# Optimization experiments

Measured on AMD Instinct MI355X. Metric: run time of the kernel, lower is better.

Reference implementation:

```python
import jax, jax.numpy as jnp
import numpy as np

H = 8          # head_num
DK = 16        # qkv_dim
CLIP = 10.0    # logit clipping


def _heads(x):
    # (b, n, H*DK) -> (b, H, n, DK)
    b, n, _ = x.shape
    return x.reshape(b, n, H, DK).transpose(0, 2, 1, 3)


def setup_inputs() -> dict:
    key = jax.random.key(0)
    ks = jax.random.split(key, 10)
    batch, problem, d, klen = 2048, 100, 128, 10
    s = 1.0 / np.sqrt(d)
    problems = jax.random.uniform(ks[0], (batch, problem, 2), dtype=jnp.float32)
    encoded_nodes = jax.random.normal(ks[1], (batch, problem, d), dtype=jnp.float32)
    Wq_first = jax.random.normal(ks[2], (d, H * DK), dtype=jnp.float32) * s
    Wq_last = jax.random.normal(ks[3], (d, H * DK), dtype=jnp.float32) * s
    Wk = jax.random.normal(ks[4], (d, H * DK), dtype=jnp.float32) * s
    Wv = jax.random.normal(ks[5], (d, H * DK), dtype=jnp.float32) * s
    Wcomb = jax.random.normal(ks[6], (H * DK, d), dtype=jnp.float32) * s
    # prefix: k distinct node indices per batch row (first k of a random permutation)
    perm = jax.vmap(lambda kk: jax.random.permutation(kk, problem))(
        jax.random.split(ks[7], batch))
    prefix = perm[:, :klen].astype(jnp.int32)
    return {"problems": problems, "encoded_nodes": encoded_nodes,
            "Wq_first": Wq_first, "Wq_last": Wq_last, "Wk": Wk, "Wv": Wv,
            "Wcomb": Wcomb, "prefix": prefix}


def reference(problems, encoded_nodes, Wq_first, Wq_last, Wk, Wv, Wcomb, prefix):
    batch, problem, d = encoded_nodes.shape
    b_idx = jnp.arange(batch)
    sqrt_dk = jnp.sqrt(jnp.float32(DK))
    sqrt_d = jnp.sqrt(jnp.float32(d))

    # set_kv: precompute multi-head K, V once (single-head key = encoded_nodes)
    kh = _heads(encoded_nodes @ Wk)   # (b, H, n, DK)
    vh = _heads(encoded_nodes @ Wv)   # (b, H, n, DK)

    # set_q1: query contribution of the first node (last node of prefix)
    last0 = prefix[:, -1]
    q1 = _heads(encoded_nodes[b_idx, last0][:, None, :] @ Wq_first)  # (b, H, 1, DK)

    # visited mask from prefix
    visited0 = jnp.zeros((batch, problem), dtype=bool)
    visited0 = visited0.at[b_idx[:, None], prefix].set(True)

    def step(carry, _):
        visited, cur = carry
        enc_last = encoded_nodes[b_idx, cur][:, None, :]            # (b, 1, d)
        q = q1 + _heads(enc_last @ Wq_last)                         # (b, H, 1, DK)
        ninf = jnp.where(visited, -jnp.inf, 0.0)                    # (b, n)
        scores = jnp.einsum('bhqe,bhne->bhqn', q, kh) / sqrt_dk
        att = jax.nn.softmax(scores + ninf[:, None, None, :], axis=-1)
        mh = jnp.einsum('bhqn,bhne->bhqe', att, vh)                 # (b, H, 1, DK)
        mh = mh.transpose(0, 2, 1, 3).reshape(batch, 1, H * DK) @ Wcomb  # (b, 1, d)
        sc = jnp.einsum('bqd,bnd->bqn', mh, encoded_nodes)[:, 0] / sqrt_d  # (b, n)
        logits = CLIP * jnp.tanh(sc) + ninf
        sel = jnp.argmax(logits, axis=-1)                           # (b,)
        visited = visited.at[b_idx, sel].set(True)
        return (visited, sel), sel

    steps = problem - prefix.shape[1]
    _, sels = jax.lax.scan(step, (visited0, last0), None, length=steps)
    tour = jnp.concatenate([prefix, sels.T.astype(prefix.dtype)], axis=1)  # (b, problem)
    return tour
```

## Files before the change

### kernel.cpp

```cpp
#include <hip/hip_runtime.h>
#include <math.h>

#define N      100
#define D      128
#define KL     10
#define S0     90
#define STEPS  90
#define LDK    132
#define NT     512

__device__ __forceinline__ float dot4(float4 a, float4 b) {
  return a.x*b.x + a.y*b.y + a.z*b.z + a.w*b.w;
}
__device__ __forceinline__ void fma4(float4& acc, float a, float4 v) {
  acc.x += a*v.x; acc.y += a*v.y; acc.z += a*v.z; acc.w += a*v.w;
}

template<int RPT>
__device__ __forceinline__ void cc(const float* __restrict__ encB,
                                   const float* __restrict__ W,
                                   bool wRowMajor, int base, int cnt,
                                   const int* __restrict__ slotNode,
                                   float* __restrict__ stage, int tid) {
  const int col = tid & 127;
  const int grp = tid >> 7;
  float acc[RPT];
  int   nd [RPT];
  #pragma unroll
  for (int ii = 0; ii < RPT; ++ii) {
    acc[ii] = 0.f;
    int r = grp + 4*ii;
    nd[ii] = (r < cnt) ? __builtin_amdgcn_readfirstlane(slotNode[base + r]) : 0;
  }
  for (int dd = 0; dd < D; dd += 16) {
    float w[16];
    #pragma unroll
    for (int t = 0; t < 16; ++t)
      w[t] = wRowMajor ? W[col*D + dd + t] : W[(dd+t)*D + col];
    #pragma unroll
    for (int ii = 0; ii < RPT; ++ii) {
      int r = grp + 4*ii;
      if (r < cnt) {
        const float* er = encB + (size_t)nd[ii]*D + dd;
        float a0=0,a1=0,a2=0,a3=0;
        #pragma unroll
        for (int t = 0; t < 16; t += 4) {
          a0 += er[t]*w[t];   a1 += er[t+1]*w[t+1];
          a2 += er[t+2]*w[t+2]; a3 += er[t+3]*w[t+3];
        }
        acc[ii] += (a0+a1)+(a2+a3);
      }
    }
  }
  #pragma unroll
  for (int ii = 0; ii < RPT; ++ii) {
    int r = grp + 4*ii;
    if (r < cnt) stage[(base + r)*LDK + col] = acc[ii];
  }
}

__global__ __launch_bounds__(NT, 4)
void policy_kernel(const float* __restrict__ enc,
                   const float* __restrict__ Wq_first,
                   const float* __restrict__ Wq_last,
                   const float* __restrict__ Wk,
                   const float* __restrict__ Wv,
                   const float* __restrict__ Wcomb,
                   const int*   __restrict__ prefix,
                   int*         __restrict__ out) {
  __shared__ __align__(16) float sCE[S0*LDK];
  __shared__ __align__(16) float sq[D];
  __shared__ __align__(16) float sAtt[8*96];
  __shared__ __align__(16) float sMh[D];
  __shared__ float sSum[8];
  __shared__ int   sSlotNode[96];
  __shared__ unsigned long long sPacked[2];
  __shared__ int   sLast0;

  const int tid = threadIdx.x;
  const int b   = blockIdx.x;
  const float* encB = enc + (size_t)b*N*D;

  if (tid < KL) out[(size_t)b*N + tid] = prefix[b*KL + tid];
  if (tid < 48) sAtt[(tid/6)*96 + 90 + (tid%6)] = 0.f;
  if (tid == 0) {
    unsigned vis[4] = {0u,0u,0u,0u};
    const int* pr = prefix + b*KL;
    for (int j = 0; j < KL; ++j) { int n = pr[j]; vis[n>>5] |= 1u << (n&31); }
    int cnt = 0;
    for (int n = 0; n < N; ++n)
      if (!((vis[n>>5] >> (n&31)) & 1u)) sSlotNode[cnt++] = n;
    sLast0 = pr[KL-1];
    sPacked[0] = 0ull; sPacked[1] = 0ull;
  }
  __syncthreads();

  if (tid < D) {
    const int last0 = sLast0;
    const float* er = encB + (size_t)last0*D;
    float a0=0,a1=0,a2=0,a3=0;
    #pragma unroll
    for (int d = 0; d < D; d += 4) {
      a0 += er[d]  *Wq_first[d*D     + tid];
      a1 += er[d+1]*Wq_first[(d+1)*D + tid];
      a2 += er[d+2]*Wq_first[(d+2)*D + tid];
      a3 += er[d+3]*Wq_first[(d+3)*D + tid];
    }
    sMh[tid] = (a0+a1)+(a2+a3);
  }
  __syncthreads();

  const int col = tid & 127;
  const int grp = tid >> 7;
  float qp[23];
  {
    int nd[23];
    #pragma unroll
    for (int ii = 0; ii < 23; ++ii) {
      int r = grp + 4*ii;
      nd[ii] = (r < S0) ? __builtin_amdgcn_readfirstlane(sSlotNode[r])
                        : ((r == S0) ? sLast0 : 0);
      qp[ii] = 0.f;
    }
    for (int dd = 0; dd < D; dd += 16) {
      float w[16];
      #pragma unroll
      for (int t = 0; t < 16; ++t) w[t] = Wq_last[(dd+t)*D + col];
      #pragma unroll
      for (int ii = 0; ii < 23; ++ii) {
        int r = grp + 4*ii;
        if (r <= S0) {
          const float* er = encB + (size_t)nd[ii]*D + dd;
          float a0=0,a1=0,a2=0,a3=0;
          #pragma unroll
          for (int t = 0; t < 16; t += 4) {
            a0 += er[t]*w[t];   a1 += er[t+1]*w[t+1];
            a2 += er[t+2]*w[t+2]; a3 += er[t+3]*w[t+3];
          }
          qp[ii] += (a0+a1)+(a2+a3);
        }
      }
    }
    const float q1c = sMh[col];
    #pragma unroll
    for (int ii = 0; ii < 23; ++ii) qp[ii] += q1c;
  }

  const int h = tid >> 6, l = tid & 63;

  cc<23>(encB, Wk, false, 0, S0, sSlotNode, sCE, tid);
  __syncthreads();
  float4 ka0,ka1,ka2,ka3, kb0,kb1,kb2,kb3;
  {
    const float* p = &sCE[l*LDK + h*16];
    ka0 = *(const float4*)(p+0);  ka1 = *(const float4*)(p+4);
    ka2 = *(const float4*)(p+8);  ka3 = *(const float4*)(p+12);
  }
  if (l < 26) {
    const float* p = &sCE[(64+l)*LDK + h*16];
    kb0 = *(const float4*)(p+0);  kb1 = *(const float4*)(p+4);
    kb2 = *(const float4*)(p+8);  kb3 = *(const float4*)(p+12);
  } else {
    kb0=kb1=kb2=kb3 = make_float4(0.f,0.f,0.f,0.f);
  }
  __syncthreads();

  const int cQuad = tid >> 4;
  const int cStrm = tid & 15;
  const int ch    = cQuad >> 2;
  cc<12>(encB, Wv, false,  0, 48, sSlotNode, sCE, tid);
  cc<12>(encB, Wv, false, 48, 42, sSlotNode, sCE, tid);
  __syncthreads();
  float4 v0,v1,v2,v3,v4,v5;
  v0 = *(const float4*)&sCE[(cStrm     )*LDK + cQuad*4];
  v1 = *(const float4*)&sCE[(cStrm + 16)*LDK + cQuad*4];
  v2 = *(const float4*)&sCE[(cStrm + 32)*LDK + cQuad*4];
  v3 = *(const float4*)&sCE[(cStrm + 48)*LDK + cQuad*4];
  v4 = *(const float4*)&sCE[(cStrm + 64)*LDK + cQuad*4];
  v5 = (cStrm < 10) ? *(const float4*)&sCE[(cStrm + 80)*LDK + cQuad*4]
                    : make_float4(0.f,0.f,0.f,0.f);
  __syncthreads();

  cc<6>(encB, Wcomb, true,  0, 24, sSlotNode, sCE, tid);
  cc<6>(encB, Wcomb, true, 24, 24, sSlotNode, sCE, tid);
  cc<6>(encB, Wcomb, true, 48, 24, sSlotNode, sCE, tid);
  cc<6>(encB, Wcomb, true, 72, 18, sSlotNode, sCE, tid);
  if (grp == 2) sq[col] = qp[22];
  __syncthreads();

  const int di  = tid >> 2;
  const int dkc = tid & 3;
  float visA = 0.f, visB = 0.f, visD = 0.f;

  for (int step = 0; step < STEPS; ++step) {
    const int p = step & 1;

    {
      if (tid == NT-1) sPacked[p] = 0ull;
      const float4 q0 = *(const float4*)&sq[h*16 + 0];
      const float4 q1 = *(const float4*)&sq[h*16 + 4];
      const float4 q2 = *(const float4*)&sq[h*16 + 8];
      const float4 q3 = *(const float4*)&sq[h*16 + 12];
      float s0 = dot4(q0,ka0)+dot4(q1,ka1)+dot4(q2,ka2)+dot4(q3,ka3);
      float x0 = expf(s0*0.25f + visA);
      sAtt[h*96 + l] = x0;
      float x1 = 0.f;
      if (l < 26) {
        float s1 = dot4(q0,kb0)+dot4(q1,kb1)+dot4(q2,kb2)+dot4(q3,kb3);
        x1 = expf(s1*0.25f + visB);
        sAtt[h*96 + 64 + l] = x1;
      }
      float loc = x0 + x1;
      #pragma unroll
      for (int off = 32; off; off >>= 1) loc += __shfl_xor(loc, off);
      if (l == 0) sSum[h] = loc;
    }
    __syncthreads();

    {
      float4 acc = make_float4(0.f,0.f,0.f,0.f);
      fma4(acc, sAtt[ch*96 + cStrm     ], v0);
      fma4(acc, sAtt[ch*96 + cStrm + 16], v1);
      fma4(acc, sAtt[ch*96 + cStrm + 32], v2);
      fma4(acc, sAtt[ch*96 + cStrm + 48], v3);
      fma4(acc, sAtt[ch*96 + cStrm + 64], v4);
      fma4(acc, sAtt[ch*96 + cStrm + 80], v5);
      #pragma unroll
      for (int off = 1; off < 16; off <<= 1) {
        acc.x += __shfl_xor(acc.x, off);
        acc.y += __shfl_xor(acc.y, off);
        acc.z += __shfl_xor(acc.z, off);
        acc.w += __shfl_xor(acc.w, off);
      }
      if (cStrm == 0) {
        const float r = 1.0f / sSum[ch];
        float4 o; o.x=acc.x*r; o.y=acc.y*r; o.z=acc.z*r; o.w=acc.w*r;
        *(float4*)&sMh[cQuad*4] = o;
      }
    }
    __syncthreads();

    if (tid < 384) {
      float a = 0.f;
      #pragma unroll
      for (int j = 0; j < 8; ++j) {
        const float4 ce = *(const float4*)&sCE[di*LDK + dkc*32 + j*4];
        const float4 mh = *(const float4*)&sMh[dkc*32 + j*4];
        a += dot4(ce, mh);
      }
      a += __shfl_xor(a, 1);
      a += __shfl_xor(a, 2);
      float val = (di < S0) ? a + visD : -INFINITY;
      int   idx = (di < S0) ? di : 127;
      #pragma unroll
      for (int off = 32; off; off >>= 1) {
        float ov = __shfl_xor(val, off);
        int   oi = __shfl_xor(idx, off);
        if (ov > val || (ov == val && oi < idx)) { val = ov; idx = oi; }
      }
      if (l == 0) {
        unsigned s = __float_as_uint(val);
        s = (s & 0x80000000u) ? ~s : (s | 0x80000000u);
        unsigned long long pk = ((unsigned long long)s << 32)
                              | (unsigned long long)(unsigned)(127 - idx);
        atomicMax(&sPacked[p], pk);
      }
    }
    __syncthreads();

    {
      const unsigned long long u = sPacked[p];
      const int idx = __builtin_amdgcn_readfirstlane(127 - (int)(u & 0xFFull));
      if (tid == 0) out[(size_t)b*N + KL + step] = sSlotNode[idx];
      if (idx == l)      visA = -INFINITY;
      if (idx == l + 64) visB = -INFINITY;
      if (idx == di)     visD = -INFINITY;
      const int want = idx >> 2;
      float qv = qp[0];
      #pragma unroll
      for (int ii = 1; ii < 23; ++ii) qv = (want == ii) ? qp[ii] : qv;
      if (grp == (idx & 3)) sq[col] = qv;
    }
    __syncthreads();
  }
}

extern "C" void kernel_launch(void* const* d_in, const int* in_sizes, int n_in,
                              void* d_out, int out_size, void* d_ws, size_t ws_size,
                              hipStream_t stream) {
  const float* enc      = (const float*)d_in[1];
  const float* Wq_first = (const float*)d_in[2];
  const float* Wq_last  = (const float*)d_in[3];
  const float* Wk       = (const float*)d_in[4];
  const float* Wv       = (const float*)d_in[5];
  const float* Wcomb    = (const float*)d_in[6];
  const int*   prefix   = (const int*)d_in[7];
  const int batch = in_sizes[7] / KL;
  policy_kernel<<<batch, NT, 0, stream>>>(enc, Wq_first, Wq_last, Wk, Wv, Wcomb,
                                          prefix, (int*)d_out);
}
```

Before: 2.567 ms.

## Remap query ownership per wavefront and drop two block barriers per step

Query-projection columns are reassigned so that each wavefront computes and updates exactly the 16 query entries of its own head. The attention-weight sum and the query refresh can then rely on ordering within a wavefront, which removes the barrier after the softmax and the barrier at the end of each step. The reset of the argmax slot moves to the next step's buffer, the argmax shuffle skips lane offsets that are already reduced, and the select chain over saved queries becomes a switch. The cost is a dependence on intra-wave LDS ordering with no explicit fence, and a switch that may compile to branches or indexed register access.

```diff
diff --git a/kernel.cpp b/kernel.cpp
--- a/kernel.cpp
+++ b/kernel.cpp
@@ -110,25 +110,26 @@
   }
   __syncthreads();
 
-  const int col = tid & 127;
-  const int grp = tid >> 7;
+  const int h = tid >> 6, l = tid & 63;
+
+  const int qcol = (h << 4) | (l & 15);
+  const int qrg  = l >> 4;
   float qp[23];
   {
     int nd[23];
     #pragma unroll
     for (int ii = 0; ii < 23; ++ii) {
-      int r = grp + 4*ii;
-      nd[ii] = (r < S0) ? __builtin_amdgcn_readfirstlane(sSlotNode[r])
-                        : ((r == S0) ? sLast0 : 0);
+      int r = qrg + 4*ii;
+      nd[ii] = (r < S0) ? sSlotNode[r] : ((r == S0) ? sLast0 : 0);
       qp[ii] = 0.f;
     }
     for (int dd = 0; dd < D; dd += 16) {
       float w[16];
       #pragma unroll
-      for (int t = 0; t < 16; ++t) w[t] = Wq_last[(dd+t)*D + col];
+      for (int t = 0; t < 16; ++t) w[t] = Wq_last[(dd+t)*D + qcol];
       #pragma unroll
       for (int ii = 0; ii < 23; ++ii) {
-        int r = grp + 4*ii;
+        int r = qrg + 4*ii;
         if (r <= S0) {
           const float* er = encB + (size_t)nd[ii]*D + dd;
           float a0=0,a1=0,a2=0,a3=0;
@@ -141,12 +142,10 @@
         }
       }
     }
-    const float q1c = sMh[col];
+    const float q1c = sMh[qcol];
     #pragma unroll
     for (int ii = 0; ii < 23; ++ii) qp[ii] += q1c;
   }
-
-  const int h = tid >> 6, l = tid & 63;
 
   cc<23>(encB, Wk, false, 0, S0, sSlotNode, sCE, tid);
   __syncthreads();
@@ -185,7 +184,7 @@
   cc<6>(encB, Wcomb, true, 24, 24, sSlotNode, sCE, tid);
   cc<6>(encB, Wcomb, true, 48, 24, sSlotNode, sCE, tid);
   cc<6>(encB, Wcomb, true, 72, 18, sSlotNode, sCE, tid);
-  if (grp == 2) sq[col] = qp[22];
+  if (qrg == 2) sq[qcol] = qp[22];
   __syncthreads();
 
   const int di  = tid >> 2;
@@ -193,10 +192,7 @@
   float visA = 0.f, visB = 0.f, visD = 0.f;
 
   for (int step = 0; step < STEPS; ++step) {
-    const int p = step & 1;
-
     {
-      if (tid == NT-1) sPacked[p] = 0ull;
       const float4 q0 = *(const float4*)&sq[h*16 + 0];
       const float4 q1 = *(const float4*)&sq[h*16 + 4];
       const float4 q2 = *(const float4*)&sq[h*16 + 8];
@@ -215,7 +211,6 @@
       for (int off = 32; off; off >>= 1) loc += __shfl_xor(loc, off);
       if (l == 0) sSum[h] = loc;
     }
-    __syncthreads();
 
     {
       float4 acc = make_float4(0.f,0.f,0.f,0.f);
@@ -240,6 +235,8 @@
     }
     __syncthreads();
 
+    if (tid == NT-1) sPacked[(step+1)&1] = 0ull;
+
     if (tid < 384) {
       float a = 0.f;
       #pragma unroll
@@ -253,7 +250,7 @@
       float val = (di < S0) ? a + visD : -INFINITY;
       int   idx = (di < S0) ? di : 127;
       #pragma unroll
-      for (int off = 32; off; off >>= 1) {
+      for (int off = 4; off <= 32; off <<= 1) {
         float ov = __shfl_xor(val, off);
         int   oi = __shfl_xor(idx, off);
         if (ov > val || (ov == val && oi < idx)) { val = ov; idx = oi; }
@@ -263,25 +260,47 @@
         s = (s & 0x80000000u) ? ~s : (s | 0x80000000u);
         unsigned long long pk = ((unsigned long long)s << 32)
                               | (unsigned long long)(unsigned)(127 - idx);
-        atomicMax(&sPacked[p], pk);
+        atomicMax(&sPacked[step&1], pk);
       }
     }
     __syncthreads();
 
     {
-      const unsigned long long u = sPacked[p];
+      const unsigned long long u = sPacked[step & 1];
       const int idx = __builtin_amdgcn_readfirstlane(127 - (int)(u & 0xFFull));
       if (tid == 0) out[(size_t)b*N + KL + step] = sSlotNode[idx];
       if (idx == l)      visA = -INFINITY;
       if (idx == l + 64) visB = -INFINITY;
       if (idx == di)     visD = -INFINITY;
       const int want = idx >> 2;
-      float qv = qp[0];
-      #pragma unroll
-      for (int ii = 1; ii < 23; ++ii) qv = (want == ii) ? qp[ii] : qv;
-      if (grp == (idx & 3)) sq[col] = qv;
-    }
-    __syncthreads();
+      float qv;
+      switch (want) {
+        case  0: qv = qp[ 0]; break;
+        case  1: qv = qp[ 1]; break;
+        case  2: qv = qp[ 2]; break;
+        case  3: qv = qp[ 3]; break;
+        case  4: qv = qp[ 4]; break;
+        case  5: qv = qp[ 5]; break;
+        case  6: qv = qp[ 6]; break;
+        case  7: qv = qp[ 7]; break;
+        case  8: qv = qp[ 8]; break;
+        case  9: qv = qp[ 9]; break;
+        case 10: qv = qp[10]; break;
+        case 11: qv = qp[11]; break;
+        case 12: qv = qp[12]; break;
+        case 13: qv = qp[13]; break;
+        case 14: qv = qp[14]; break;
+        case 15: qv = qp[15]; break;
+        case 16: qv = qp[16]; break;
+        case 17: qv = qp[17]; break;
+        case 18: qv = qp[18]; break;
+        case 19: qv = qp[19]; break;
+        case 20: qv = qp[20]; break;
+        case 21: qv = qp[21]; break;
+        default: qv = qp[22]; break;
+      }
+      if (qrg == (idx & 3)) sq[qcol] = qv;
+    }
   }
 }
 
```

New measurement: 7.373 ms. +187.2%, slower.

## Remap per-head query ownership to drop two block barriers per decode step

Applied to the files above, without the earlier changes.

Query rows are now staged through shared memory and redistributed so each wave holds the query columns of its own attention head. The per-step score, attention-V and query-update phases then only touch data produced by the same wave, which lets two of the four per-step __syncthreads be removed. The sPacked reset moves to the next buffer, and the argmax shuffle skips offsets already reduced. This adds a one-time shared-memory round trip at setup, and correctness now rests on the exact wave-to-head mapping.

```diff
diff --git a/kernel.cpp b/kernel.cpp
--- a/kernel.cpp
+++ b/kernel.cpp
@@ -110,17 +110,18 @@
   }
   __syncthreads();
 
-  const int col = tid & 127;
-  const int grp = tid >> 7;
-  float qp[23];
+  const int h = tid >> 6, l = tid & 63;
+
   {
-    int nd[23];
+    const int col = tid & 127;
+    const int grp = tid >> 7;
+    float acc[23]; int nd[23];
     #pragma unroll
     for (int ii = 0; ii < 23; ++ii) {
       int r = grp + 4*ii;
+      acc[ii] = 0.f;
       nd[ii] = (r < S0) ? __builtin_amdgcn_readfirstlane(sSlotNode[r])
                         : ((r == S0) ? sLast0 : 0);
-      qp[ii] = 0.f;
     }
     for (int dd = 0; dd < D; dd += 16) {
       float w[16];
@@ -137,16 +138,31 @@
             a0 += er[t]*w[t];   a1 += er[t+1]*w[t+1];
             a2 += er[t+2]*w[t+2]; a3 += er[t+3]*w[t+3];
           }
-          qp[ii] += (a0+a1)+(a2+a3);
+          acc[ii] += (a0+a1)+(a2+a3);
         }
       }
     }
-    const float q1c = sMh[col];
-    #pragma unroll
-    for (int ii = 0; ii < 23; ++ii) qp[ii] += q1c;
-  }
-
-  const int h = tid >> 6, l = tid & 63;
+    #pragma unroll
+    for (int ii = 0; ii < 23; ++ii) {
+      int r = grp + 4*ii;
+      if (r < S0)       sCE[r*LDK + col] = acc[ii];
+      else if (r == S0) sq[col] = acc[ii] + sMh[col];
+    }
+  }
+  __syncthreads();
+
+  const int qcol = (h << 4) | (l & 15);
+  const int qrg  = l >> 4;
+  float qp[23];
+  {
+    const float q1c = sMh[qcol];
+    #pragma unroll
+    for (int ii = 0; ii < 23; ++ii) {
+      int r = qrg + 4*ii;
+      qp[ii] = (r < S0) ? (sCE[r*LDK + qcol] + q1c) : 0.f;
+    }
+  }
+  __syncthreads();
 
   cc<23>(encB, Wk, false, 0, S0, sSlotNode, sCE, tid);
   __syncthreads();
@@ -185,7 +201,6 @@
   cc<6>(encB, Wcomb, true, 24, 24, sSlotNode, sCE, tid);
   cc<6>(encB, Wcomb, true, 48, 24, sSlotNode, sCE, tid);
   cc<6>(encB, Wcomb, true, 72, 18, sSlotNode, sCE, tid);
-  if (grp == 2) sq[col] = qp[22];
   __syncthreads();
 
   const int di  = tid >> 2;
@@ -193,10 +208,7 @@
   float visA = 0.f, visB = 0.f, visD = 0.f;
 
   for (int step = 0; step < STEPS; ++step) {
-    const int p = step & 1;
-
     {
-      if (tid == NT-1) sPacked[p] = 0ull;
       const float4 q0 = *(const float4*)&sq[h*16 + 0];
       const float4 q1 = *(const float4*)&sq[h*16 + 4];
       const float4 q2 = *(const float4*)&sq[h*16 + 8];
@@ -215,7 +227,6 @@
       for (int off = 32; off; off >>= 1) loc += __shfl_xor(loc, off);
       if (l == 0) sSum[h] = loc;
     }
-    __syncthreads();
 
     {
       float4 acc = make_float4(0.f,0.f,0.f,0.f);
@@ -240,6 +251,8 @@
     }
     __syncthreads();
 
+    if (tid == NT-1) sPacked[(step+1)&1] = 0ull;
+
     if (tid < 384) {
       float a = 0.f;
       #pragma unroll
@@ -253,7 +266,7 @@
       float val = (di < S0) ? a + visD : -INFINITY;
       int   idx = (di < S0) ? di : 127;
       #pragma unroll
-      for (int off = 32; off; off >>= 1) {
+      for (int off = 4; off <= 32; off <<= 1) {
         float ov = __shfl_xor(val, off);
         int   oi = __shfl_xor(idx, off);
         if (ov > val || (ov == val && oi < idx)) { val = ov; idx = oi; }
@@ -263,13 +276,13 @@
         s = (s & 0x80000000u) ? ~s : (s | 0x80000000u);
         unsigned long long pk = ((unsigned long long)s << 32)
                               | (unsigned long long)(unsigned)(127 - idx);
-        atomicMax(&sPacked[p], pk);
+        atomicMax(&sPacked[step&1], pk);
       }
     }
     __syncthreads();
 
     {
-      const unsigned long long u = sPacked[p];
+      const unsigned long long u = sPacked[step & 1];
       const int idx = __builtin_amdgcn_readfirstlane(127 - (int)(u & 0xFFull));
       if (tid == 0) out[(size_t)b*N + KL + step] = sSlotNode[idx];
       if (idx == l)      visA = -INFINITY;
@@ -279,9 +292,8 @@
       float qv = qp[0];
       #pragma unroll
       for (int ii = 1; ii < 23; ++ii) qv = (want == ii) ? qp[ii] : qv;
-      if (grp == (idx & 3)) sq[col] = qv;
-    }
-    __syncthreads();
+      if (qrg == (idx & 3)) sq[qcol] = qv;
+    }
   }
 }
 
```

Result: faster. 2.482 ms (-3.3%).
